# Kernel optimization log

Hardware: AMD Instinct MI355X
Metric: run time of the kernel (lower is better)

The kernel has to match this reference:

```python
import jax, jax.numpy as jnp
import numpy as np

N_NODES = 100000
N_EDGES = 1600000
D_IN = 64


def _graph_conv(x, edge_src, edge_dst, W, b, n_nodes):
    # gather source features along edges, mean-aggregate at destinations,
    # then linear transform + ReLU (standard GraphConv semantics)
    msgs = x[edge_src]  # [E, d]
    agg = jax.ops.segment_sum(msgs, edge_dst, num_segments=n_nodes)  # [N, d]
    deg = jax.ops.segment_sum(jnp.ones((edge_src.shape[0],), x.dtype), edge_dst,
                              num_segments=n_nodes)  # [N]
    agg = agg / jnp.maximum(deg, 1.0)[:, None]
    return jax.nn.relu(agg @ W + b)


def setup_inputs() -> dict:
    key = jax.random.key(0)
    ks = jax.random.split(key, 6)
    node_features = jax.random.normal(ks[0], (N_NODES, D_IN), dtype=jnp.float32)
    edge_src = jax.random.randint(ks[1], (N_EDGES,), 0, N_NODES)
    edge_dst = jax.random.randint(ks[2], (N_EDGES,), 0, N_NODES)
    W1 = jax.random.normal(ks[3], (D_IN, 64), dtype=jnp.float32) * (1.0 / np.sqrt(D_IN))
    b1 = jnp.zeros((64,), jnp.float32)
    W2 = jax.random.normal(ks[4], (64, 32), dtype=jnp.float32) * (1.0 / np.sqrt(64))
    b2 = jnp.zeros((32,), jnp.float32)
    Wd = jax.random.normal(ks[5], (1, 1), dtype=jnp.float32)
    bd = jnp.zeros((1,), jnp.float32)
    return {"node_features": node_features, "edge_src": edge_src, "edge_dst": edge_dst,
            "W1": W1, "b1": b1, "W2": W2, "b2": b2, "Wd": Wd, "bd": bd}


def reference(node_features, edge_src, edge_dst, W1, b1, W2, b2, Wd, bd):
    n_nodes = node_features.shape[0]
    x = _graph_conv(node_features, edge_src, edge_dst, W1, b1, n_nodes)  # [N, 64]
    x = _graph_conv(x, edge_src, edge_dst, W2, b2, n_nodes)              # [N, 32]
    x = jnp.mean(x, axis=1, keepdims=True)                               # [N, 1]
    return jax.nn.sigmoid(x @ Wd + bd)                                   # [N, 1]
```

## Files before the change

kernel.cpp:

```cpp
#include <hip/hip_runtime.h>
#include <hip/hip_bf16.h>

#define N_NODES 100000
#define N_EDGES 1600000
#define N_PAD   100096
#define BSHIFT  10
#define NBUCKET 98
#define BCAP    19456
#define EPB     4096
#define ZROW1   N_NODES
#define ZROW2   (2 * N_NODES)

__device__ __forceinline__ unsigned short f32_to_bf16(float f) {
    unsigned int u = __float_as_uint(f);
    unsigned int r = (u + 0x7fffu + ((u >> 16) & 1u)) >> 16;
    return (unsigned short)r;
}
__device__ __forceinline__ float bf16_lo(unsigned int p) {
    return __uint_as_float(p << 16);
}
__device__ __forceinline__ float bf16_hi(unsigned int p) {
    return __uint_as_float(p & 0xffff0000u);
}

__global__ void __launch_bounds__(256) bucket_scatter_lds(
    const int* __restrict__ src, const int* __restrict__ dst,
    int* __restrict__ bcur, unsigned int* __restrict__ tmp, int n_edges) {
    __shared__ int lh[128];
    int t = threadIdx.x;
    int e0 = blockIdx.x * EPB;
    int e1 = min(e0 + EPB, n_edges);
    if (t < 128) lh[t] = 0;
    __syncthreads();
    int ls[16], ld[16];
    #pragma unroll
    for (int j = 0; j < 16; j++) {
        int e = e0 + t + j * 256;
        if (e < e1) {
            ls[j] = src[e];
            ld[j] = dst[e];
            atomicAdd(&lh[ld[j] >> BSHIFT], 1);
        }
    }
    __syncthreads();
    if (t < NBUCKET) {
        int c = lh[t];
        lh[t] = (c > 0) ? atomicAdd(&bcur[t], c) : 0;
    }
    __syncthreads();
    #pragma unroll
    for (int j = 0; j < 16; j++) {
        int e = e0 + t + j * 256;
        if (e < e1) {
            int b = ld[j] >> BSHIFT;
            int p = atomicAdd(&lh[b], 1);
            if (p < BCAP)
                tmp[(size_t)b * BCAP + p] =
                    ((unsigned)ls[j] << BSHIFT) | (unsigned)(ld[j] & 1023);
        }
    }
}

__global__ void __launch_bounds__(1024) bucket_to_csr(
    const unsigned int* __restrict__ tmp, const int* __restrict__ bcur,
    int2* __restrict__ meta, int* __restrict__ col, int n_nodes) {
    __shared__ int nh[1024];
    __shared__ int npref[1024];
    int b = blockIdx.x;
    int t = threadIdx.x;
    int m = min(bcur[b], BCAP);
    int cbase = b * BCAP;
    nh[t] = 0;
    __syncthreads();
    const unsigned int* te = tmp + (size_t)b * BCAP;
    for (int i = t; i < m; i += 1024) atomicAdd(&nh[te[i] & 1023], 1);
    __syncthreads();
    npref[t] = nh[t];
    __syncthreads();
    for (int off = 1; off < 1024; off <<= 1) {
        int u = (t >= off) ? npref[t - off] : 0;
        __syncthreads();
        npref[t] += u;
        __syncthreads();
    }
    int node = (b << BSHIFT) + t;
    int ex = npref[t] - nh[t];
    if (node < n_nodes) meta[node] = make_int2(cbase + ex, nh[t]);
    nh[t] = cbase + ex;
    __syncthreads();
    for (int i = t; i < m; i += 1024) {
        unsigned int e = te[i];
        int pos = atomicAdd(&nh[e & 1023], 1);
        col[pos] = (int)(e >> BSHIFT);
    }
}

__global__ void __launch_bounds__(256) gemm_n64(const float4* __restrict__ X4,
                                                const float* __restrict__ W,
                                                unsigned short* __restrict__ Y, int M) {
    __shared__ float sx[64][65];
    __shared__ float sw[64 * 64];
    int t = threadIdx.x;
    int base = blockIdx.x * 64;
    for (int i = t; i < 64 * 16; i += 256) {
        int r = i >> 4, c4 = i & 15;
        int row = base + r;
        float4 v = make_float4(0.f, 0.f, 0.f, 0.f);
        if (row < M) v = X4[(size_t)row * 16 + c4];
        sx[r][c4 * 4 + 0] = v.x; sx[r][c4 * 4 + 1] = v.y;
        sx[r][c4 * 4 + 2] = v.z; sx[r][c4 * 4 + 3] = v.w;
    }
    float4* sw4 = (float4*)sw;
    const float4* W4 = (const float4*)W;
    for (int i = t; i < 64 * 16; i += 256) sw4[i] = W4[i];
    __syncthreads();

    int tm = t & 15;
    int tn = t >> 4;
    float acc[4][4] = {{0.f}};
    #pragma unroll 8
    for (int k = 0; k < 64; k++) {
        float4 b = sw4[k * 16 + tn];
        float a0 = sx[tm * 4 + 0][k], a1 = sx[tm * 4 + 1][k];
        float a2 = sx[tm * 4 + 2][k], a3 = sx[tm * 4 + 3][k];
        acc[0][0] = fmaf(a0, b.x, acc[0][0]); acc[0][1] = fmaf(a0, b.y, acc[0][1]);
        acc[0][2] = fmaf(a0, b.z, acc[0][2]); acc[0][3] = fmaf(a0, b.w, acc[0][3]);
        acc[1][0] = fmaf(a1, b.x, acc[1][0]); acc[1][1] = fmaf(a1, b.y, acc[1][1]);
        acc[1][2] = fmaf(a1, b.z, acc[1][2]); acc[1][3] = fmaf(a1, b.w, acc[1][3]);
        acc[2][0] = fmaf(a2, b.x, acc[2][0]); acc[2][1] = fmaf(a2, b.y, acc[2][1]);
        acc[2][2] = fmaf(a2, b.z, acc[2][2]); acc[2][3] = fmaf(a2, b.w, acc[2][3]);
        acc[3][0] = fmaf(a3, b.x, acc[3][0]); acc[3][1] = fmaf(a3, b.y, acc[3][1]);
        acc[3][2] = fmaf(a3, b.z, acc[3][2]); acc[3][3] = fmaf(a3, b.w, acc[3][3]);
    }
    #pragma unroll
    for (int i = 0; i < 4; i++) {
        int row = base + tm * 4 + i;
        if (row < M) {
            ushort4 p;
            p.x = f32_to_bf16(acc[i][0]); p.y = f32_to_bf16(acc[i][1]);
            p.z = f32_to_bf16(acc[i][2]); p.w = f32_to_bf16(acc[i][3]);
            *(ushort4*)&Y[(size_t)row * 64 + tn * 4] = p;
        }
    }
}

__global__ void __launch_bounds__(256) gemm_n32(const float4* __restrict__ X4,
                                                const float* __restrict__ W,
                                                unsigned short* __restrict__ Z, int M) {
    __shared__ float sx[128][65];
    __shared__ float sw[64 * 32];
    int t = threadIdx.x;
    int base = blockIdx.x * 128;
    for (int i = t; i < 128 * 16; i += 256) {
        int r = i >> 4, c4 = i & 15;
        int row = base + r;
        float4 v = make_float4(0.f, 0.f, 0.f, 0.f);
        if (row < M) v = X4[(size_t)row * 16 + c4];
        sx[r][c4 * 4 + 0] = v.x; sx[r][c4 * 4 + 1] = v.y;
        sx[r][c4 * 4 + 2] = v.z; sx[r][c4 * 4 + 3] = v.w;
    }
    float4* sw4 = (float4*)sw;
    const float4* W4 = (const float4*)W;
    for (int i = t; i < 64 * 8; i += 256) sw4[i] = W4[i];
    __syncthreads();

    int tm = t & 31;
    int tn = t >> 5;
    float acc[4][4] = {{0.f}};
    #pragma unroll 8
    for (int k = 0; k < 64; k++) {
        float4 b = sw4[k * 8 + tn];
        float a0 = sx[tm * 4 + 0][k], a1 = sx[tm * 4 + 1][k];
        float a2 = sx[tm * 4 + 2][k], a3 = sx[tm * 4 + 3][k];
        acc[0][0] = fmaf(a0, b.x, acc[0][0]); acc[0][1] = fmaf(a0, b.y, acc[0][1]);
        acc[0][2] = fmaf(a0, b.z, acc[0][2]); acc[0][3] = fmaf(a0, b.w, acc[0][3]);
        acc[1][0] = fmaf(a1, b.x, acc[1][0]); acc[1][1] = fmaf(a1, b.y, acc[1][1]);
        acc[1][2] = fmaf(a1, b.z, acc[1][2]); acc[1][3] = fmaf(a1, b.w, acc[1][3]);
        acc[2][0] = fmaf(a2, b.x, acc[2][0]); acc[2][1] = fmaf(a2, b.y, acc[2][1]);
        acc[2][2] = fmaf(a2, b.z, acc[2][2]); acc[2][3] = fmaf(a2, b.w, acc[2][3]);
        acc[3][0] = fmaf(a3, b.x, acc[3][0]); acc[3][1] = fmaf(a3, b.y, acc[3][1]);
        acc[3][2] = fmaf(a3, b.z, acc[3][2]); acc[3][3] = fmaf(a3, b.w, acc[3][3]);
    }
    #pragma unroll
    for (int i = 0; i < 4; i++) {
        int row = base + tm * 4 + i;
        if (row < M) {
            ushort4 p;
            p.x = f32_to_bf16(acc[i][0]); p.y = f32_to_bf16(acc[i][1]);
            p.z = f32_to_bf16(acc[i][2]); p.w = f32_to_bf16(acc[i][3]);
            *(ushort4*)&Z[(size_t)row * 32 + tn * 4] = p;
        }
    }
}

__global__ void __launch_bounds__(256) gather_relu64(
    const uint4* __restrict__ Y4, const int2* __restrict__ meta,
    const int* __restrict__ col, const float* __restrict__ b1,
    float4* __restrict__ H4, int n_nodes) {
    int n = blockIdx.x * 4 + (threadIdx.x >> 6);
    if (n >= n_nodes) return;
    int lane = threadIdx.x & 63;
    int g = lane >> 3;
    int c = lane & 7;
    int2 md = meta[n];
    int beg = md.x;
    int d = md.y;
    int dm1 = max(d - 1, 0);

    float acc[8] = {0.f, 0.f, 0.f, 0.f, 0.f, 0.f, 0.f, 0.f};
    for (int i = 0; i < d; i += 32) {
        int i0 = i + g;
        int i1 = i0 + 8;
        int i2 = i0 + 16;
        int i3 = i0 + 24;
        int t0 = col[beg + min(i0, dm1)];
        int t1 = col[beg + min(i1, dm1)];
        int t2 = col[beg + min(i2, dm1)];
        int t3 = col[beg + min(i3, dm1)];
        int s0 = (i0 < d) ? t0 : ZROW1;
        int s1 = (i1 < d) ? t1 : ZROW1;
        int s2 = (i2 < d) ? t2 : ZROW1;
        int s3 = (i3 < d) ? t3 : ZROW1;
        uint4 v0 = Y4[(size_t)s0 * 8 + c];
        uint4 v1 = Y4[(size_t)s1 * 8 + c];
        uint4 v2 = Y4[(size_t)s2 * 8 + c];
        uint4 v3 = Y4[(size_t)s3 * 8 + c];
        acc[0] += (bf16_lo(v0.x) + bf16_lo(v1.x)) + (bf16_lo(v2.x) + bf16_lo(v3.x));
        acc[1] += (bf16_hi(v0.x) + bf16_hi(v1.x)) + (bf16_hi(v2.x) + bf16_hi(v3.x));
        acc[2] += (bf16_lo(v0.y) + bf16_lo(v1.y)) + (bf16_lo(v2.y) + bf16_lo(v3.y));
        acc[3] += (bf16_hi(v0.y) + bf16_hi(v1.y)) + (bf16_hi(v2.y) + bf16_hi(v3.y));
        acc[4] += (bf16_lo(v0.z) + bf16_lo(v1.z)) + (bf16_lo(v2.z) + bf16_lo(v3.z));
        acc[5] += (bf16_hi(v0.z) + bf16_hi(v1.z)) + (bf16_hi(v2.z) + bf16_hi(v3.z));
        acc[6] += (bf16_lo(v0.w) + bf16_lo(v1.w)) + (bf16_lo(v2.w) + bf16_lo(v3.w));
        acc[7] += (bf16_hi(v0.w) + bf16_hi(v1.w)) + (bf16_hi(v2.w) + bf16_hi(v3.w));
    }
    #pragma unroll
    for (int m = 8; m <= 32; m <<= 1) {
        #pragma unroll
        for (int q = 0; q < 8; q++) acc[q] += __shfl_xor(acc[q], m);
    }
    float inv = 1.0f / fmaxf((float)d, 1.0f);
    const float4* b1_4 = (const float4*)b1;
    float4 ba = b1_4[c * 2], bb = b1_4[c * 2 + 1];
    if (g == 0) {
        float4 o0, o1;
        o0.x = fmaxf(fmaf(acc[0], inv, ba.x), 0.f);
        o0.y = fmaxf(fmaf(acc[1], inv, ba.y), 0.f);
        o0.z = fmaxf(fmaf(acc[2], inv, ba.z), 0.f);
        o0.w = fmaxf(fmaf(acc[3], inv, ba.w), 0.f);
        o1.x = fmaxf(fmaf(acc[4], inv, bb.x), 0.f);
        o1.y = fmaxf(fmaf(acc[5], inv, bb.y), 0.f);
        o1.z = fmaxf(fmaf(acc[6], inv, bb.z), 0.f);
        o1.w = fmaxf(fmaf(acc[7], inv, bb.w), 0.f);
        H4[(size_t)n * 16 + c * 2]     = o0;
        H4[(size_t)n * 16 + c * 2 + 1] = o1;
    }
}

__global__ void __launch_bounds__(256) gather_final32(
    const uint4* __restrict__ Z4, const int2* __restrict__ meta,
    const int* __restrict__ col, const float* __restrict__ b2,
    const float* __restrict__ Wd, const float* __restrict__ bd,
    float* __restrict__ out, int n_nodes) {
    int n = blockIdx.x * 4 + (threadIdx.x >> 6);
    if (n >= n_nodes) return;
    int lane = threadIdx.x & 63;
    int g = lane >> 2;
    int c = lane & 3;
    int2 md = meta[n];
    int beg = md.x;
    int d = md.y;
    int dm1 = max(d - 1, 0);

    float acc[8] = {0.f, 0.f, 0.f, 0.f, 0.f, 0.f, 0.f, 0.f};
    for (int i = 0; i < d; i += 32) {
        int i0 = i + g;
        int i1 = i0 + 16;
        int t0 = col[beg + min(i0, dm1)];
        int t1 = col[beg + min(i1, dm1)];
        int s0 = (i0 < d) ? t0 : ZROW2;
        int s1 = (i1 < d) ? t1 : ZROW2;
        uint4 v0 = Z4[(size_t)s0 * 4 + c];
        uint4 v1 = Z4[(size_t)s1 * 4 + c];
        acc[0] += bf16_lo(v0.x) + bf16_lo(v1.x);
        acc[1] += bf16_hi(v0.x) + bf16_hi(v1.x);
        acc[2] += bf16_lo(v0.y) + bf16_lo(v1.y);
        acc[3] += bf16_hi(v0.y) + bf16_hi(v1.y);
        acc[4] += bf16_lo(v0.z) + bf16_lo(v1.z);
        acc[5] += bf16_hi(v0.z) + bf16_hi(v1.z);
        acc[6] += bf16_lo(v0.w) + bf16_lo(v1.w);
        acc[7] += bf16_hi(v0.w) + bf16_hi(v1.w);
    }
    #pragma unroll
    for (int m = 4; m <= 32; m <<= 1) {
        #pragma unroll
        for (int q = 0; q < 8; q++) acc[q] += __shfl_xor(acc[q], m);
    }
    float inv = 1.0f / fmaxf((float)d, 1.0f);
    const float4* b2_4 = (const float4*)b2;
    float4 ba = b2_4[c * 2], bb = b2_4[c * 2 + 1];
    float local = 0.f;
    local += fmaxf(fmaf(acc[0], inv, ba.x), 0.f);
    local += fmaxf(fmaf(acc[1], inv, ba.y), 0.f);
    local += fmaxf(fmaf(acc[2], inv, ba.z), 0.f);
    local += fmaxf(fmaf(acc[3], inv, ba.w), 0.f);
    local += fmaxf(fmaf(acc[4], inv, bb.x), 0.f);
    local += fmaxf(fmaf(acc[5], inv, bb.y), 0.f);
    local += fmaxf(fmaf(acc[6], inv, bb.z), 0.f);
    local += fmaxf(fmaf(acc[7], inv, bb.w), 0.f);
    local += __shfl_xor(local, 1);
    local += __shfl_xor(local, 2);
    if (lane == 0) {
        float z = fmaf(local * (1.0f / 32.0f), Wd[0], bd[0]);
        out[n] = 1.0f / (1.0f + __expf(-z));
    }
}

extern "C" void kernel_launch(void* const* d_in, const int* in_sizes, int n_in,
                              void* d_out, int out_size, void* d_ws, size_t ws_size,
                              hipStream_t stream) {
    const float* x    = (const float*)d_in[0];
    const int*   esrc = (const int*)d_in[1];
    const int*   edst = (const int*)d_in[2];
    const float* W1   = (const float*)d_in[3];
    const float* b1   = (const float*)d_in[4];
    const float* W2   = (const float*)d_in[5];
    const float* b2   = (const float*)d_in[6];
    const float* Wd   = (const float*)d_in[7];
    const float* bd   = (const float*)d_in[8];
    float* out = (float*)d_out;

    int*  bcur = (int*)d_ws;
    int2* meta = (int2*)(bcur + 128);
    int*  col  = (int*)(meta + N_PAD);
    float* h   = (float*)(col + (size_t)NBUCKET * BCAP + 64);
    unsigned int* tmp = (unsigned int*)h;
    unsigned short* y  = (unsigned short*)(h + (size_t)N_NODES * 64);
    unsigned short* z2 = y;

    hipMemsetAsync((void*)bcur, 0, 128 * sizeof(int), stream);
    hipMemsetAsync((void*)(y + (size_t)N_NODES * 64), 0, 128, stream);

    bucket_scatter_lds<<<(N_EDGES + EPB - 1) / EPB, 256, 0, stream>>>(
        esrc, edst, bcur, tmp, N_EDGES);
    bucket_to_csr<<<NBUCKET, 1024, 0, stream>>>(tmp, bcur, meta, col, N_NODES);

    gemm_n64<<<(N_NODES + 63) / 64, 256, 0, stream>>>((const float4*)x, W1, y, N_NODES);
    gather_relu64<<<(N_NODES + 3) / 4, 256, 0, stream>>>(
        (const uint4*)y, meta, col, b1, (float4*)h, N_NODES);
    gemm_n32<<<(N_NODES + 127) / 128, 256, 0, stream>>>((const float4*)h, W2, z2, N_NODES);
    gather_final32<<<(N_NODES + 3) / 4, 256, 0, stream>>>(
        (const uint4*)z2, meta, col, b2, Wd, bd, out, N_NODES);
}
```

Before: 241.2 us.

## Split bucket-to-CSR into per-window blocks for more parallelism

Replaces the 98-block, 1024-thread CSR build with 784 blocks of 256 threads. Each block owns a 128-node window of a bucket and scans the whole bucket, keeping only its window's edges. This puts many more blocks on the GPU's compute units and shortens the prefix scans, at the cost of each bucket being read eight times and a per-window capacity cap (WCAP) that could drop edges if a window overflows.

```diff
diff --git a/kernel.cpp b/kernel.cpp
--- a/kernel.cpp
+++ b/kernel.cpp
@@ -8,6 +8,10 @@
 #define NBUCKET 98
 #define BCAP    19456
 #define EPB     4096
+#define WSHIFT  7
+#define NWIN    8
+#define WCAP    2432
+#define NWBLK   (NBUCKET * NWIN)
 #define ZROW1   N_NODES
 #define ZROW2   (2 * N_NODES)
 
@@ -61,37 +65,49 @@
     }
 }
 
-__global__ void __launch_bounds__(1024) bucket_to_csr(
+__global__ void __launch_bounds__(256) place_window(
     const unsigned int* __restrict__ tmp, const int* __restrict__ bcur,
     int2* __restrict__ meta, int* __restrict__ col, int n_nodes) {
-    __shared__ int nh[1024];
-    __shared__ int npref[1024];
-    int b = blockIdx.x;
-    int t = threadIdx.x;
-    int m = min(bcur[b], BCAP);
-    int cbase = b * BCAP;
-    nh[t] = 0;
-    __syncthreads();
+    __shared__ int hist[128];
+    __shared__ int pref[128];
+    int wb = blockIdx.x;
+    int b  = wb >> 3;
+    int w  = wb & 7;
+    int t  = threadIdx.x;
+    int m  = min(bcur[b], BCAP);
     const unsigned int* te = tmp + (size_t)b * BCAP;
-    for (int i = t; i < m; i += 1024) atomicAdd(&nh[te[i] & 1023], 1);
-    __syncthreads();
-    npref[t] = nh[t];
-    __syncthreads();
-    for (int off = 1; off < 1024; off <<= 1) {
-        int u = (t >= off) ? npref[t - off] : 0;
+    if (t < 128) hist[t] = 0;
+    __syncthreads();
+    for (int i = t; i < m; i += 256) {
+        unsigned int r = te[i];
+        int dl = (int)(r & 1023);
+        if ((dl >> WSHIFT) == w) atomicAdd(&hist[dl & 127], 1);
+    }
+    __syncthreads();
+    if (t < 128) pref[t] = hist[t];
+    __syncthreads();
+    for (int off = 1; off < 128; off <<= 1) {
+        int u = (t < 128 && t >= off) ? pref[t - off] : 0;
         __syncthreads();
-        npref[t] += u;
+        if (t < 128) pref[t] += u;
         __syncthreads();
     }
-    int node = (b << BSHIFT) + t;
-    int ex = npref[t] - nh[t];
-    if (node < n_nodes) meta[node] = make_int2(cbase + ex, nh[t]);
-    nh[t] = cbase + ex;
-    __syncthreads();
-    for (int i = t; i < m; i += 1024) {
-        unsigned int e = te[i];
-        int pos = atomicAdd(&nh[e & 1023], 1);
-        col[pos] = (int)(e >> BSHIFT);
+    int wbase = wb * WCAP;
+    if (t < 128) {
+        int node = (b << BSHIFT) + (w << WSHIFT) + t;
+        int ex = pref[t] - hist[t];
+        if (node < n_nodes) meta[node] = make_int2(wbase + ex, hist[t]);
+        hist[t] = wbase + ex;
+    }
+    __syncthreads();
+    int wlim = wbase + WCAP;
+    for (int i = t; i < m; i += 256) {
+        unsigned int r = te[i];
+        int dl = (int)(r & 1023);
+        if ((dl >> WSHIFT) == w) {
+            int pos = atomicAdd(&hist[dl & 127], 1);
+            if (pos < wlim) col[pos] = (int)(r >> BSHIFT);
+        }
     }
 }
 
@@ -333,7 +349,7 @@
     int*  bcur = (int*)d_ws;
     int2* meta = (int2*)(bcur + 128);
     int*  col  = (int*)(meta + N_PAD);
-    float* h   = (float*)(col + (size_t)NBUCKET * BCAP + 64);
+    float* h   = (float*)(col + (size_t)NWBLK * WCAP + 64);
     unsigned int* tmp = (unsigned int*)h;
     unsigned short* y  = (unsigned short*)(h + (size_t)N_NODES * 64);
     unsigned short* z2 = y;
@@ -343,7 +359,7 @@
 
     bucket_scatter_lds<<<(N_EDGES + EPB - 1) / EPB, 256, 0, stream>>>(
         esrc, edst, bcur, tmp, N_EDGES);
-    bucket_to_csr<<<NBUCKET, 1024, 0, stream>>>(tmp, bcur, meta, col, N_NODES);
+    place_window<<<NWBLK, 256, 0, stream>>>(tmp, bcur, meta, col, N_NODES);
 
     gemm_n64<<<(N_NODES + 63) / 64, 256, 0, stream>>>((const float4*)x, W1, y, N_NODES);
     gather_relu64<<<(N_NODES + 3) / 4, 256, 0, stream>>>(
```

Measured after the change: 273.8 us. 13.5% more time.

## Fuse edge scatter with first GEMM and pad CSR rows to 32

Applied to the files above, without the earlier changes.

The edge bucket-scatter and the first dense GEMM now run as one launch, with block index choosing the role, so the two independent stages can overlap and one launch goes away. CSR rows are padded to a multiple of 32 with a zero-row index, which removes the per-edge bounds clamps and selects in both gather kernels. GEMMs now write the zero row themselves, and z2 gets its own buffer, so the separate memset is dropped. The cost is larger col storage, extra padding writes in bucket_to_csr, and a shared-memory footprint sized for the GEMM role that also applies to scatter blocks.

```diff
diff --git a/kernel.cpp b/kernel.cpp
--- a/kernel.cpp
+++ b/kernel.cpp
@@ -8,8 +8,10 @@
 #define NBUCKET 98
 #define BCAP    19456
 #define EPB     4096
-#define ZROW1   N_NODES
-#define ZROW2   (2 * N_NODES)
+#define NSCAT   391
+#define NGEMM1  1563
+#define PCAP    34816
+#define ZROW    N_NODES
 
 __device__ __forceinline__ unsigned short f32_to_bf16(float f) {
     unsigned int u = __float_as_uint(f);
@@ -23,40 +25,89 @@
     return __uint_as_float(p & 0xffff0000u);
 }
 
-__global__ void __launch_bounds__(256) bucket_scatter_lds(
+__global__ void __launch_bounds__(256) k1_scatter_gemm64(
     const int* __restrict__ src, const int* __restrict__ dst,
-    int* __restrict__ bcur, unsigned int* __restrict__ tmp, int n_edges) {
-    __shared__ int lh[128];
+    int* __restrict__ bcur, unsigned int* __restrict__ tmp,
+    const float4* __restrict__ X4, const float* __restrict__ W,
+    unsigned short* __restrict__ Y, int n_edges, int M) {
+    extern __shared__ char smem[];
     int t = threadIdx.x;
-    int e0 = blockIdx.x * EPB;
-    int e1 = min(e0 + EPB, n_edges);
-    if (t < 128) lh[t] = 0;
-    __syncthreads();
-    int ls[16], ld[16];
+    if (blockIdx.x < NSCAT) {
+        int* lh = (int*)smem;
+        int e0 = blockIdx.x * EPB;
+        int e1 = min(e0 + EPB, n_edges);
+        if (t < 128) lh[t] = 0;
+        __syncthreads();
+        int ls[16], ld[16];
+        #pragma unroll
+        for (int j = 0; j < 16; j++) {
+            int e = e0 + t + j * 256;
+            if (e < e1) {
+                ls[j] = src[e];
+                ld[j] = dst[e];
+                atomicAdd(&lh[ld[j] >> BSHIFT], 1);
+            }
+        }
+        __syncthreads();
+        if (t < NBUCKET) {
+            int c = lh[t];
+            lh[t] = (c > 0) ? atomicAdd(&bcur[t], c) : 0;
+        }
+        __syncthreads();
+        #pragma unroll
+        for (int j = 0; j < 16; j++) {
+            int e = e0 + t + j * 256;
+            if (e < e1) {
+                int b = ld[j] >> BSHIFT;
+                int p = atomicAdd(&lh[b], 1);
+                if (p < BCAP)
+                    tmp[(size_t)b * BCAP + p] =
+                        ((unsigned)ls[j] << BSHIFT) | (unsigned)(ld[j] & 1023);
+            }
+        }
+        return;
+    }
+    float* sx = (float*)smem;
+    float* sw = sx + 64 * 65;
+    int base = (blockIdx.x - NSCAT) * 64;
+    for (int i = t; i < 64 * 16; i += 256) {
+        int r = i >> 4, c4 = i & 15;
+        int row = base + r;
+        float4 v = make_float4(0.f, 0.f, 0.f, 0.f);
+        if (row < M) v = X4[(size_t)row * 16 + c4];
+        sx[r * 65 + c4 * 4 + 0] = v.x; sx[r * 65 + c4 * 4 + 1] = v.y;
+        sx[r * 65 + c4 * 4 + 2] = v.z; sx[r * 65 + c4 * 4 + 3] = v.w;
+    }
+    float4* sw4 = (float4*)sw;
+    const float4* W4 = (const float4*)W;
+    for (int i = t; i < 64 * 16; i += 256) sw4[i] = W4[i];
+    __syncthreads();
+
+    int tm = t & 15;
+    int tn = t >> 4;
+    float acc[4][4] = {{0.f}};
+    #pragma unroll 8
+    for (int k = 0; k < 64; k++) {
+        float4 b = sw4[k * 16 + tn];
+        float a0 = sx[(tm * 4 + 0) * 65 + k], a1 = sx[(tm * 4 + 1) * 65 + k];
+        float a2 = sx[(tm * 4 + 2) * 65 + k], a3 = sx[(tm * 4 + 3) * 65 + k];
+        acc[0][0] = fmaf(a0, b.x, acc[0][0]); acc[0][1] = fmaf(a0, b.y, acc[0][1]);
+        acc[0][2] = fmaf(a0, b.z, acc[0][2]); acc[0][3] = fmaf(a0, b.w, acc[0][3]);
+        acc[1][0] = fmaf(a1, b.x, acc[1][0]); acc[1][1] = fmaf(a1, b.y, acc[1][1]);
+        acc[1][2] = fmaf(a1, b.z, acc[1][2]); acc[1][3] = fmaf(a1, b.w, acc[1][3]);
+        acc[2][0] = fmaf(a2, b.x, acc[2][0]); acc[2][1] = fmaf(a2, b.y, acc[2][1]);
+        acc[2][2] = fmaf(a2, b.z, acc[2][2]); acc[2][3] = fmaf(a2, b.w, acc[2][3]);
+        acc[3][0] = fmaf(a3, b.x, acc[3][0]); acc[3][1] = fmaf(a3, b.y, acc[3][1]);
+        acc[3][2] = fmaf(a3, b.z, acc[3][2]); acc[3][3] = fmaf(a3, b.w, acc[3][3]);
+    }
     #pragma unroll
-    for (int j = 0; j < 16; j++) {
-        int e = e0 + t + j * 256;
-        if (e < e1) {
-            ls[j] = src[e];
-            ld[j] = dst[e];
-            atomicAdd(&lh[ld[j] >> BSHIFT], 1);
-        }
-    }
-    __syncthreads();
-    if (t < NBUCKET) {
-        int c = lh[t];
-        lh[t] = (c > 0) ? atomicAdd(&bcur[t], c) : 0;
-    }
-    __syncthreads();
-    #pragma unroll
-    for (int j = 0; j < 16; j++) {
-        int e = e0 + t + j * 256;
-        if (e < e1) {
-            int b = ld[j] >> BSHIFT;
-            int p = atomicAdd(&lh[b], 1);
-            if (p < BCAP)
-                tmp[(size_t)b * BCAP + p] =
-                    ((unsigned)ls[j] << BSHIFT) | (unsigned)(ld[j] & 1023);
+    for (int i = 0; i < 4; i++) {
+        int row = base + tm * 4 + i;
+        if (row <= M) {
+            ushort4 p;
+            p.x = f32_to_bf16(acc[i][0]); p.y = f32_to_bf16(acc[i][1]);
+            p.z = f32_to_bf16(acc[i][2]); p.w = f32_to_bf16(acc[i][3]);
+            *(ushort4*)&Y[(size_t)row * 64 + tn * 4] = p;
         }
     }
 }
@@ -69,13 +120,15 @@
     int b = blockIdx.x;
     int t = threadIdx.x;
     int m = min(bcur[b], BCAP);
-    int cbase = b * BCAP;
+    int cbase = b * PCAP;
     nh[t] = 0;
     __syncthreads();
     const unsigned int* te = tmp + (size_t)b * BCAP;
     for (int i = t; i < m; i += 1024) atomicAdd(&nh[te[i] & 1023], 1);
     __syncthreads();
-    npref[t] = nh[t];
+    int d  = nh[t];
+    int pc = (d + 31) & ~31;
+    npref[t] = pc;
     __syncthreads();
     for (int off = 1; off < 1024; off <<= 1) {
         int u = (t >= off) ? npref[t - off] : 0;
@@ -83,64 +136,16 @@
         npref[t] += u;
         __syncthreads();
     }
+    int begin = cbase + npref[t] - pc;
     int node = (b << BSHIFT) + t;
-    int ex = npref[t] - nh[t];
-    if (node < n_nodes) meta[node] = make_int2(cbase + ex, nh[t]);
-    nh[t] = cbase + ex;
+    if (node < n_nodes) meta[node] = make_int2(begin, d);
+    for (int j = d; j < pc; j++) col[begin + j] = ZROW;
+    nh[t] = begin;
     __syncthreads();
     for (int i = t; i < m; i += 1024) {
         unsigned int e = te[i];
         int pos = atomicAdd(&nh[e & 1023], 1);
         col[pos] = (int)(e >> BSHIFT);
-    }
-}
-
-__global__ void __launch_bounds__(256) gemm_n64(const float4* __restrict__ X4,
-                                                const float* __restrict__ W,
-                                                unsigned short* __restrict__ Y, int M) {
-    __shared__ float sx[64][65];
-    __shared__ float sw[64 * 64];
-    int t = threadIdx.x;
-    int base = blockIdx.x * 64;
-    for (int i = t; i < 64 * 16; i += 256) {
-        int r = i >> 4, c4 = i & 15;
-        int row = base + r;
-        float4 v = make_float4(0.f, 0.f, 0.f, 0.f);
-        if (row < M) v = X4[(size_t)row * 16 + c4];
-        sx[r][c4 * 4 + 0] = v.x; sx[r][c4 * 4 + 1] = v.y;
-        sx[r][c4 * 4 + 2] = v.z; sx[r][c4 * 4 + 3] = v.w;
-    }
-    float4* sw4 = (float4*)sw;
-    const float4* W4 = (const float4*)W;
-    for (int i = t; i < 64 * 16; i += 256) sw4[i] = W4[i];
-    __syncthreads();
-
-    int tm = t & 15;
-    int tn = t >> 4;
-    float acc[4][4] = {{0.f}};
-    #pragma unroll 8
-    for (int k = 0; k < 64; k++) {
-        float4 b = sw4[k * 16 + tn];
-        float a0 = sx[tm * 4 + 0][k], a1 = sx[tm * 4 + 1][k];
-        float a2 = sx[tm * 4 + 2][k], a3 = sx[tm * 4 + 3][k];
-        acc[0][0] = fmaf(a0, b.x, acc[0][0]); acc[0][1] = fmaf(a0, b.y, acc[0][1]);
-        acc[0][2] = fmaf(a0, b.z, acc[0][2]); acc[0][3] = fmaf(a0, b.w, acc[0][3]);
-        acc[1][0] = fmaf(a1, b.x, acc[1][0]); acc[1][1] = fmaf(a1, b.y, acc[1][1]);
-        acc[1][2] = fmaf(a1, b.z, acc[1][2]); acc[1][3] = fmaf(a1, b.w, acc[1][3]);
-        acc[2][0] = fmaf(a2, b.x, acc[2][0]); acc[2][1] = fmaf(a2, b.y, acc[2][1]);
-        acc[2][2] = fmaf(a2, b.z, acc[2][2]); acc[2][3] = fmaf(a2, b.w, acc[2][3]);
-        acc[3][0] = fmaf(a3, b.x, acc[3][0]); acc[3][1] = fmaf(a3, b.y, acc[3][1]);
-        acc[3][2] = fmaf(a3, b.z, acc[3][2]); acc[3][3] = fmaf(a3, b.w, acc[3][3]);
-    }
-    #pragma unroll
-    for (int i = 0; i < 4; i++) {
-        int row = base + tm * 4 + i;
-        if (row < M) {
-            ushort4 p;
-            p.x = f32_to_bf16(acc[i][0]); p.y = f32_to_bf16(acc[i][1]);
-            p.z = f32_to_bf16(acc[i][2]); p.w = f32_to_bf16(acc[i][3]);
-            *(ushort4*)&Y[(size_t)row * 64 + tn * 4] = p;
-        }
     }
 }
 
@@ -184,7 +189,7 @@
     #pragma unroll
     for (int i = 0; i < 4; i++) {
         int row = base + tm * 4 + i;
-        if (row < M) {
+        if (row <= M) {
             ushort4 p;
             p.x = f32_to_bf16(acc[i][0]); p.y = f32_to_bf16(acc[i][1]);
             p.z = f32_to_bf16(acc[i][2]); p.w = f32_to_bf16(acc[i][3]);
@@ -205,22 +210,13 @@
     int2 md = meta[n];
     int beg = md.x;
     int d = md.y;
-    int dm1 = max(d - 1, 0);
 
     float acc[8] = {0.f, 0.f, 0.f, 0.f, 0.f, 0.f, 0.f, 0.f};
     for (int i = 0; i < d; i += 32) {
-        int i0 = i + g;
-        int i1 = i0 + 8;
-        int i2 = i0 + 16;
-        int i3 = i0 + 24;
-        int t0 = col[beg + min(i0, dm1)];
-        int t1 = col[beg + min(i1, dm1)];
-        int t2 = col[beg + min(i2, dm1)];
-        int t3 = col[beg + min(i3, dm1)];
-        int s0 = (i0 < d) ? t0 : ZROW1;
-        int s1 = (i1 < d) ? t1 : ZROW1;
-        int s2 = (i2 < d) ? t2 : ZROW1;
-        int s3 = (i3 < d) ? t3 : ZROW1;
+        int s0 = col[beg + i + g];
+        int s1 = col[beg + i + g + 8];
+        int s2 = col[beg + i + g + 16];
+        int s3 = col[beg + i + g + 24];
         uint4 v0 = Y4[(size_t)s0 * 8 + c];
         uint4 v1 = Y4[(size_t)s1 * 8 + c];
         uint4 v2 = Y4[(size_t)s2 * 8 + c];
@@ -270,16 +266,11 @@
     int2 md = meta[n];
     int beg = md.x;
     int d = md.y;
-    int dm1 = max(d - 1, 0);
 
     float acc[8] = {0.f, 0.f, 0.f, 0.f, 0.f, 0.f, 0.f, 0.f};
     for (int i = 0; i < d; i += 32) {
-        int i0 = i + g;
-        int i1 = i0 + 16;
-        int t0 = col[beg + min(i0, dm1)];
-        int t1 = col[beg + min(i1, dm1)];
-        int s0 = (i0 < d) ? t0 : ZROW2;
-        int s1 = (i1 < d) ? t1 : ZROW2;
+        int s0 = col[beg + i + g];
+        int s1 = col[beg + i + g + 16];
         uint4 v0 = Z4[(size_t)s0 * 4 + c];
         uint4 v1 = Z4[(size_t)s1 * 4 + c];
         acc[0] += bf16_lo(v0.x) + bf16_lo(v1.x);
@@ -333,19 +324,16 @@
     int*  bcur = (int*)d_ws;
     int2* meta = (int2*)(bcur + 128);
     int*  col  = (int*)(meta + N_PAD);
-    float* h   = (float*)(col + (size_t)NBUCKET * BCAP + 64);
+    float* h   = (float*)(col + (size_t)NBUCKET * PCAP + 1024);
     unsigned int* tmp = (unsigned int*)h;
     unsigned short* y  = (unsigned short*)(h + (size_t)N_NODES * 64);
-    unsigned short* z2 = y;
+    unsigned short* z2 = y + (size_t)(N_NODES + 1) * 64;
 
     hipMemsetAsync((void*)bcur, 0, 128 * sizeof(int), stream);
-    hipMemsetAsync((void*)(y + (size_t)N_NODES * 64), 0, 128, stream);
-
-    bucket_scatter_lds<<<(N_EDGES + EPB - 1) / EPB, 256, 0, stream>>>(
-        esrc, edst, bcur, tmp, N_EDGES);
+
+    k1_scatter_gemm64<<<NSCAT + NGEMM1, 256, 33024, stream>>>(
+        esrc, edst, bcur, tmp, (const float4*)x, W1, y, N_EDGES, N_NODES);
     bucket_to_csr<<<NBUCKET, 1024, 0, stream>>>(tmp, bcur, meta, col, N_NODES);
-
-    gemm_n64<<<(N_NODES + 63) / 64, 256, 0, stream>>>((const float4*)x, W1, y, N_NODES);
     gather_relu64<<<(N_NODES + 3) / 4, 256, 0, stream>>>(
         (const uint4*)y, meta, col, b1, (float4*)h, N_NODES);
     gemm_n32<<<(N_NODES + 127) / 128, 256, 0, stream>>>((const float4*)h, W2, z2, N_NODES);
```

Result: no change. 237.5 us (-1.5%).
